# Performance work log

Hardware: AMD Instinct MI355X
Metric: run time of the kernel (lower is better)

Reference implementation:

```python
import jax, jax.numpy as jnp
import numpy as np

D = 256          # input_size
RNN = 256        # rnn_hidden
COND = 64        # cond_dim
HID = 128        # MLP hidden
N_FIXED = 128    # mask.sum() with alternating mask
N_FREE = D - N_FIXED
B = 131072

# Static index arrays implementing the boolean mask (even indices fixed).
IDX_FIXED = np.arange(0, D, 2)
IDX_FREE = np.arange(1, D, 2)


def setup_inputs() -> dict:
    key = jax.random.key(0)
    ks = jax.random.split(key, 8)
    in_dim = N_FIXED + RNN + COND  # 448
    x = jax.random.normal(ks[0], (B, D), jnp.float32)
    h = jax.random.normal(ks[1], (B, RNN + COND), jnp.float32)
    W1 = jax.random.normal(ks[2], (in_dim, HID), jnp.float32) / np.sqrt(in_dim)
    b1 = jnp.zeros((HID,), jnp.float32)
    W2 = jax.random.normal(ks[3], (HID, HID), jnp.float32) / np.sqrt(HID)
    b2 = jnp.zeros((HID,), jnp.float32)
    W3 = jax.random.normal(ks[4], (HID, N_FREE * 2), jnp.float32) / np.sqrt(HID)
    b3 = jnp.zeros((N_FREE * 2,), jnp.float32)
    return {"x": x, "h": h, "W1": W1, "b1": b1, "W2": W2, "b2": b2, "W3": W3, "b3": b3}


def reference(x, h, W1, b1, W2, b2, W3, b3):
    # gather fixed / free halves (static index gather == boolean-mask select)
    x_fixed = x[:, IDX_FIXED]          # [B, N_FIXED]
    x_free = x[:, IDX_FREE]            # [B, N_FREE]
    z = jnp.concatenate([x_fixed, h], axis=-1)  # [B, 448]
    a = jax.nn.relu(z @ W1 + b1)
    a = jax.nn.relu(a @ W2 + b2)
    st = a @ W3 + b3                   # [B, 2*N_FREE]
    s = jnp.tanh(st[:, :N_FREE])
    t = st[:, N_FREE:]
    y_free = x_free * jnp.exp(s) + t
    log_det = jnp.sum(s, axis=-1)
    # scatter-write back into output layout
    y = jnp.zeros_like(x).at[:, IDX_FIXED].set(x_fixed).at[:, IDX_FREE].set(y_free)
    return y, log_det
```

## Files before the change

kernel.cpp:

```cpp
#include <hip/hip_runtime.h>
#include <hip/hip_bf16.h>
#include <stdint.h>

typedef __attribute__((ext_vector_type(8))) short bf16x8;
typedef __attribute__((ext_vector_type(4))) float f32x4;

#define B_ROWS 131072
#define BM 16
#define NT 16
#define GRID 512

#define XB 16384
#define HB 20480
#define H_OFF 32768
#define A1_OFF 73728
#define LSUM_OFF 78080
#define LDS_TOTAL 78336
#define AP 136

#define W1P_OFF 0
#define W2P_OFF 7168
#define W3P_OFF 9216

typedef const __attribute__((address_space(1))) unsigned int gu32;
typedef __attribute__((address_space(3))) unsigned int lu32;

__device__ inline void gl_lds16(const void* g, void* l) {
  __builtin_amdgcn_global_load_lds((gu32*)g, (lu32*)l, 16, 0, 0);
}

__device__ inline uint16_t f2bf(float x) {
  uint32_t u = __float_as_uint(x);
  u += 0x7fffu + ((u >> 16) & 1u);
  return (uint16_t)(u >> 16);
}

__device__ inline float tanh_fast(float x) {
  x = fminf(fmaxf(x, -15.f), 15.f);
  float e = __expf(2.f * x);
  return (e - 1.f) / (e + 1.f);
}

__global__ void prepack_kernel(const float* __restrict__ W1,
                               const float* __restrict__ W2,
                               const float* __restrict__ W3,
                               uint4* __restrict__ wp) {
  int tid = blockIdx.x * 256 + threadIdx.x;
  if (tid >= 13312) return;
  int l = tid & 63, f = tid >> 6;
  const float* W; int N, kt, nt;
  if (f < 112)      { W = W1; N = 128; int ff = f;       nt = ff / 14; kt = ff - nt * 14; }
  else if (f < 144) { W = W2; N = 128; int ff = f - 112; nt = ff >> 2; kt = ff & 3; }
  else              { W = W3; N = 256; int ff = f - 144; nt = ff >> 2; kt = ff & 3; }
  int k0  = kt * 32 + (l >> 4) * 8;
  int col = nt * 16 + (l & 15);
  uint16_t v[8];
#pragma unroll
  for (int j = 0; j < 8; j++) v[j] = f2bf(W[(size_t)(k0 + j) * N + col]);
  uint4 o;
  o.x = (uint32_t)v[0] | ((uint32_t)v[1] << 16);
  o.y = (uint32_t)v[2] | ((uint32_t)v[3] << 16);
  o.z = (uint32_t)v[4] | ((uint32_t)v[5] << 16);
  o.w = (uint32_t)v[6] | ((uint32_t)v[7] << 16);
  wp[tid] = o;
}

__global__ __launch_bounds__(256, 2) void fused_kernel(
    const float* __restrict__ x, const float* __restrict__ h,
    const float* __restrict__ b1, const float* __restrict__ b2,
    const float* __restrict__ b3, const uint4* __restrict__ wp,
    float* __restrict__ y, float* __restrict__ ldet) {
  extern __shared__ uint8_t smem[];
  uint16_t* a1   = (uint16_t*)(smem + A1_OFF);
  float*    lsum = (float*)(smem + LSUM_OFF);

  const int t = threadIdx.x;
  const int wid = t >> 6, l = t & 63;
  const int lr = l & 15, lq = l >> 4;
  const int tile0 = blockIdx.x * NT;

  int xoff[4], hoff[5];
#pragma unroll
  for (int k = 0; k < 4; k++) {
    int r = wid * 4 + k;
    int c = (l & ~15) | ((l & 15) ^ (r & 15));
    xoff[k] = r * 256 + c * 4;
  }
#pragma unroll
  for (int k = 0; k < 5; k++) {
    int s = (wid * 5 + k) * 64 + l;
    int r = s / 80, cp = s - r * 80;
    int c = (cp & ~15) | ((cp & 15) ^ (r & 15));
    hoff[k] = r * 320 + c * 4;
  }

  {
    const float* xg = x + (size_t)(tile0 * BM) * 256;
    const float* hg = h + (size_t)(tile0 * BM) * 320;
#pragma unroll
    for (int k = 0; k < 4; k++)
      gl_lds16(xg + xoff[k], smem + (wid * 4 + k) * 1024);
#pragma unroll
    for (int k = 0; k < 5; k++)
      gl_lds16(hg + hoff[k], smem + H_OFF + (wid * 5 + k) * 1024);
  }

  int cur = 0;
  for (int it = 0; it < NT; ++it) {
    const int m0 = (tile0 + it) * BM;
    __syncthreads();

    const uint8_t* xsc = smem + cur * XB;
    const uint8_t* hsc = smem + H_OFF + cur * HB;
    uint16_t* a2 = (uint16_t*)(smem + H_OFF + cur * HB);

    if (it + 1 < NT) {
      const float* xg = x + (size_t)(m0 + BM) * 256;
      const float* hg = h + (size_t)(m0 + BM) * 320;
      uint8_t* xd = smem + (cur ^ 1) * XB;
      uint8_t* hd = smem + H_OFF + (cur ^ 1) * HB;
#pragma unroll
      for (int k = 0; k < 4; k++)
        gl_lds16(xg + xoff[k], xd + (wid * 4 + k) * 1024);
#pragma unroll
      for (int k = 0; k < 5; k++)
        gl_lds16(hg + hoff[k], hd + (wid * 5 + k) * 1024);
    }

    {
      f32x4 acc[2] = {};
#pragma unroll
      for (int kt = 0; kt < 4; kt++) {
        union { bf16x8 v; __hip_bfloat162 h2[4]; } u;
#pragma unroll
        for (int i = 0; i < 4; i++) {
          int slot = kt * 16 + ((lq * 4 + i) ^ lr);
          float4 q = *(const float4*)(xsc + lr * 1024 + slot * 16);
          u.h2[i] = __float22bfloat162_rn(make_float2(q.x, q.z));
        }
        bf16x8 bfr0 = *(const bf16x8*)&wp[W1P_OFF + ((wid * 2 + 0) * 14 + kt) * 64 + l];
        bf16x8 bfr1 = *(const bf16x8*)&wp[W1P_OFF + ((wid * 2 + 1) * 14 + kt) * 64 + l];
        acc[0] = __builtin_amdgcn_mfma_f32_16x16x32_bf16(u.v, bfr0, acc[0], 0, 0, 0);
        acc[1] = __builtin_amdgcn_mfma_f32_16x16x32_bf16(u.v, bfr1, acc[1], 0, 0, 0);
      }
#pragma unroll 2
      for (int kh = 0; kh < 10; kh++) {
        int c0 = kh * 8 + lq * 2;
        int qd = c0 & ~15, mm = c0 & 15;
        float4 a = *(const float4*)(hsc + lr * 1280 + (qd | (mm ^ lr)) * 16);
        float4 b = *(const float4*)(hsc + lr * 1280 + (qd | ((mm + 1) ^ lr)) * 16);
        union { bf16x8 v; __hip_bfloat162 h2[4]; } u;
        u.h2[0] = __float22bfloat162_rn(make_float2(a.x, a.y));
        u.h2[1] = __float22bfloat162_rn(make_float2(a.z, a.w));
        u.h2[2] = __float22bfloat162_rn(make_float2(b.x, b.y));
        u.h2[3] = __float22bfloat162_rn(make_float2(b.z, b.w));
        int kt = kh + 4;
        bf16x8 bfr0 = *(const bf16x8*)&wp[W1P_OFF + ((wid * 2 + 0) * 14 + kt) * 64 + l];
        bf16x8 bfr1 = *(const bf16x8*)&wp[W1P_OFF + ((wid * 2 + 1) * 14 + kt) * 64 + l];
        acc[0] = __builtin_amdgcn_mfma_f32_16x16x32_bf16(u.v, bfr0, acc[0], 0, 0, 0);
        acc[1] = __builtin_amdgcn_mfma_f32_16x16x32_bf16(u.v, bfr1, acc[1], 0, 0, 0);
      }
#pragma unroll
      for (int nj = 0; nj < 2; nj++) {
        int col = wid * 32 + nj * 16 + lr;
        float bv = b1[col];
#pragma unroll
        for (int r = 0; r < 4; r++)
          a1[(lq * 4 + r) * AP + col] = f2bf(fmaxf(acc[nj][r] + bv, 0.f));
      }
    }
    __syncthreads();

    {
      f32x4 acc[2] = {};
#pragma unroll
      for (int kt = 0; kt < 4; kt++) {
        bf16x8 afr = *(const bf16x8*)&a1[lr * AP + kt * 32 + lq * 8];
        bf16x8 bfr0 = *(const bf16x8*)&wp[W2P_OFF + ((wid * 2 + 0) * 4 + kt) * 64 + l];
        bf16x8 bfr1 = *(const bf16x8*)&wp[W2P_OFF + ((wid * 2 + 1) * 4 + kt) * 64 + l];
        acc[0] = __builtin_amdgcn_mfma_f32_16x16x32_bf16(afr, bfr0, acc[0], 0, 0, 0);
        acc[1] = __builtin_amdgcn_mfma_f32_16x16x32_bf16(afr, bfr1, acc[1], 0, 0, 0);
      }
#pragma unroll
      for (int nj = 0; nj < 2; nj++) {
        int col = wid * 32 + nj * 16 + lr;
        float bv = b2[col];
#pragma unroll
        for (int r = 0; r < 4; r++)
          a2[(lq * 4 + r) * AP + col] = f2bf(fmaxf(acc[nj][r] + bv, 0.f));
      }
    }
    __syncthreads();

    f32x4 acc3[4] = {};
#pragma unroll
    for (int kt = 0; kt < 4; kt++) {
      bf16x8 afr = *(const bf16x8*)&a2[lr * AP + kt * 32 + lq * 8];
      bf16x8 bfrS0 = *(const bf16x8*)&wp[W3P_OFF + ((wid * 2 + 0) * 4 + kt) * 64 + l];
      bf16x8 bfrS1 = *(const bf16x8*)&wp[W3P_OFF + ((wid * 2 + 1) * 4 + kt) * 64 + l];
      bf16x8 bfrT0 = *(const bf16x8*)&wp[W3P_OFF + ((8 + wid * 2 + 0) * 4 + kt) * 64 + l];
      bf16x8 bfrT1 = *(const bf16x8*)&wp[W3P_OFF + ((8 + wid * 2 + 1) * 4 + kt) * 64 + l];
      acc3[0] = __builtin_amdgcn_mfma_f32_16x16x32_bf16(afr, bfrS0, acc3[0], 0, 0, 0);
      acc3[1] = __builtin_amdgcn_mfma_f32_16x16x32_bf16(afr, bfrS1, acc3[1], 0, 0, 0);
      acc3[2] = __builtin_amdgcn_mfma_f32_16x16x32_bf16(afr, bfrT0, acc3[2], 0, 0, 0);
      acc3[3] = __builtin_amdgcn_mfma_f32_16x16x32_bf16(afr, bfrT1, acc3[3], 0, 0, 0);
    }

    float lp[4] = {0.f, 0.f, 0.f, 0.f};
#pragma unroll
    for (int nj = 0; nj < 2; nj++) {
      int colc = wid * 32 + nj * 16 + lr;
      float bs = b3[colc];
      float bt = b3[128 + colc];
#pragma unroll
      for (int r = 0; r < 4; r++) {
        int lrow = lq * 4 + r;
        float sv = tanh_fast(acc3[nj][r] + bs);
        float tv = acc3[nj + 2][r] + bt;
        lp[r] += sv;
        int cch = wid * 16 + nj * 8 + (lr >> 1);
        int slot = (cch & ~15) | ((cch & 15) ^ lrow);
        const float2 xv = *(const float2*)(xsc + lrow * 1024 + slot * 16 + (lr & 1) * 8);
        float2 o;
        o.x = xv.x;
        o.y = xv.y * __expf(sv) + tv;
        *(float2*)(y + (size_t)(m0 + lrow) * 256 + 2 * colc) = o;
      }
    }

#pragma unroll
    for (int r = 0; r < 4; r++) {
      float v = lp[r];
      v += __shfl_xor(v, 1);
      v += __shfl_xor(v, 2);
      v += __shfl_xor(v, 4);
      v += __shfl_xor(v, 8);
      if (lr == 0) lsum[wid * BM + lq * 4 + r] = v;
    }
    __syncthreads();
    if (t < BM)
      ldet[m0 + t] = lsum[t] + lsum[BM + t] + lsum[2 * BM + t] + lsum[3 * BM + t];

    cur ^= 1;
  }
}

extern "C" void kernel_launch(void* const* d_in, const int* in_sizes, int n_in,
                              void* d_out, int out_size, void* d_ws, size_t ws_size,
                              hipStream_t stream) {
  const float* x  = (const float*)d_in[0];
  const float* h  = (const float*)d_in[1];
  const float* W1 = (const float*)d_in[2];
  const float* b1 = (const float*)d_in[3];
  const float* W2 = (const float*)d_in[4];
  const float* b2 = (const float*)d_in[5];
  const float* W3 = (const float*)d_in[6];
  const float* b3 = (const float*)d_in[7];
  float* y    = (float*)d_out;
  float* ldet = y + (size_t)B_ROWS * 256;
  uint4* wp   = (uint4*)d_ws;

  prepack_kernel<<<52, 256, 0, stream>>>(W1, W2, W3, wp);

  (void)hipFuncSetAttribute((const void*)fused_kernel,
                            hipFuncAttributeMaxDynamicSharedMemorySize, LDS_TOTAL);
  fused_kernel<<<GRID, 256, LDS_TOTAL, stream>>>(x, h, b1, b2, b3, wp, y, ldet);
}
```

Measured before the change: 131.1 us.

## Use 8 waves per block with register-resident weights and bf16-staged h tiles

Doubles the block to 512 threads so each wave owns a 16-column slice, and keeps its W1/W2/W3 bf16 fragments in registers instead of reloading them from global memory every tile. The h tile is no longer copied directly into LDS; threads load it, convert it to bf16 and store it into a padded layout, which halves its LDS footprint and removes the per-MFMA conversion. The x tile now uses padded rows instead of an XOR swizzle, and a2 gets its own buffer. In exchange, register pressure rises (about 26 bf16x8 fragments per lane) and the h prefetch becomes a synchronous register round trip placed after the first barrier rather than an asynchronous load.

Measured after the change: 173.0 us. 32.0% more time.

```diff
diff --git a/kernel.cpp b/kernel.cpp
--- a/kernel.cpp
+++ b/kernel.cpp
@@ -10,12 +10,15 @@
 #define NT 16
 #define GRID 512
 
-#define XB 16384
-#define HB 20480
-#define H_OFF 32768
-#define A1_OFF 73728
-#define LSUM_OFF 78080
-#define LDS_TOTAL 78336
+#define XPITCH 1040
+#define XB (16 * XPITCH)
+#define HPITCH 656
+#define HB (16 * HPITCH)
+#define H_OFF (2 * XB)
+#define A1_OFF (H_OFF + 2 * HB)
+#define A2_OFF (A1_OFF + 16 * 272)
+#define LSUM_OFF (A2_OFF + 16 * 272)
+#define LDS_TOTAL (LSUM_OFF + 128 * 4)
 #define AP 136
 
 #define W1P_OFF 0
@@ -65,13 +68,23 @@
   wp[tid] = o;
 }
 
-__global__ __launch_bounds__(256, 2) void fused_kernel(
+__device__ inline void stage_h_chunk(uint8_t* hd, const float* hg, int j) {
+  int row = j / 80, c4 = j - row * 80;
+  float4 v = *(const float4*)(hg + 4 * j);
+  uint2 p;
+  p.x = (uint32_t)f2bf(v.x) | ((uint32_t)f2bf(v.y) << 16);
+  p.y = (uint32_t)f2bf(v.z) | ((uint32_t)f2bf(v.w) << 16);
+  *(uint2*)(hd + row * HPITCH + c4 * 8) = p;
+}
+
+__global__ __launch_bounds__(512, 2) void fused_kernel(
     const float* __restrict__ x, const float* __restrict__ h,
     const float* __restrict__ b1, const float* __restrict__ b2,
     const float* __restrict__ b3, const uint4* __restrict__ wp,
     float* __restrict__ y, float* __restrict__ ldet) {
   extern __shared__ uint8_t smem[];
   uint16_t* a1   = (uint16_t*)(smem + A1_OFF);
+  uint16_t* a2   = (uint16_t*)(smem + A2_OFF);
   float*    lsum = (float*)(smem + LSUM_OFF);
 
   const int t = threadIdx.x;
@@ -79,153 +92,116 @@
   const int lr = l & 15, lq = l >> 4;
   const int tile0 = blockIdx.x * NT;
 
-  int xoff[4], hoff[5];
-#pragma unroll
-  for (int k = 0; k < 4; k++) {
-    int r = wid * 4 + k;
-    int c = (l & ~15) | ((l & 15) ^ (r & 15));
-    xoff[k] = r * 256 + c * 4;
+  bf16x8 w1[14], w2[4], w3s[4], w3t[4];
+#pragma unroll
+  for (int kt = 0; kt < 14; kt++)
+    w1[kt] = *(const bf16x8*)&wp[W1P_OFF + (wid * 14 + kt) * 64 + l];
+#pragma unroll
+  for (int kt = 0; kt < 4; kt++) {
+    w2[kt]  = *(const bf16x8*)&wp[W2P_OFF + (wid * 4 + kt) * 64 + l];
+    w3s[kt] = *(const bf16x8*)&wp[W3P_OFF + (wid * 4 + kt) * 64 + l];
+    w3t[kt] = *(const bf16x8*)&wp[W3P_OFF + ((wid + 8) * 4 + kt) * 64 + l];
   }
-#pragma unroll
-  for (int k = 0; k < 5; k++) {
-    int s = (wid * 5 + k) * 64 + l;
-    int r = s / 80, cp = s - r * 80;
-    int c = (cp & ~15) | ((cp & 15) ^ (r & 15));
-    hoff[k] = r * 320 + c * 4;
-  }
+  const int colc = wid * 16 + lr;
+  const float b1v = b1[colc], b2v = b2[colc];
+  const float b3sv = b3[colc], b3tv = b3[128 + colc];
 
   {
     const float* xg = x + (size_t)(tile0 * BM) * 256;
     const float* hg = h + (size_t)(tile0 * BM) * 320;
 #pragma unroll
-    for (int k = 0; k < 4; k++)
-      gl_lds16(xg + xoff[k], smem + (wid * 4 + k) * 1024);
-#pragma unroll
-    for (int k = 0; k < 5; k++)
-      gl_lds16(hg + hoff[k], smem + H_OFF + (wid * 5 + k) * 1024);
+    for (int k = 0; k < 2; k++) {
+      int r = wid * 2 + k;
+      gl_lds16(xg + r * 256 + l * 4, smem + r * XPITCH);
+    }
+    stage_h_chunk(smem + H_OFF, hg, t);
+    stage_h_chunk(smem + H_OFF, hg, t + 512);
+    if (t < 256) stage_h_chunk(smem + H_OFF, hg, t + 1024);
   }
 
   int cur = 0;
   for (int it = 0; it < NT; ++it) {
     const int m0 = (tile0 + it) * BM;
+    const bool pf = (it + 1 < NT);
     __syncthreads();
 
     const uint8_t* xsc = smem + cur * XB;
     const uint8_t* hsc = smem + H_OFF + cur * HB;
-    uint16_t* a2 = (uint16_t*)(smem + H_OFF + cur * HB);
-
-    if (it + 1 < NT) {
+
+    if (pf) {
       const float* xg = x + (size_t)(m0 + BM) * 256;
-      const float* hg = h + (size_t)(m0 + BM) * 320;
       uint8_t* xd = smem + (cur ^ 1) * XB;
-      uint8_t* hd = smem + H_OFF + (cur ^ 1) * HB;
-#pragma unroll
-      for (int k = 0; k < 4; k++)
-        gl_lds16(xg + xoff[k], xd + (wid * 4 + k) * 1024);
-#pragma unroll
-      for (int k = 0; k < 5; k++)
-        gl_lds16(hg + hoff[k], hd + (wid * 5 + k) * 1024);
+#pragma unroll
+      for (int k = 0; k < 2; k++) {
+        int r = wid * 2 + k;
+        gl_lds16(xg + r * 256 + l * 4, xd + r * XPITCH);
+      }
     }
 
     {
-      f32x4 acc[2] = {};
+      f32x4 acc = {};
 #pragma unroll
       for (int kt = 0; kt < 4; kt++) {
         union { bf16x8 v; __hip_bfloat162 h2[4]; } u;
 #pragma unroll
         for (int i = 0; i < 4; i++) {
-          int slot = kt * 16 + ((lq * 4 + i) ^ lr);
-          float4 q = *(const float4*)(xsc + lr * 1024 + slot * 16);
+          float4 q = *(const float4*)(xsc + lr * XPITCH + kt * 256 + lq * 64 + i * 16);
           u.h2[i] = __float22bfloat162_rn(make_float2(q.x, q.z));
         }
-        bf16x8 bfr0 = *(const bf16x8*)&wp[W1P_OFF + ((wid * 2 + 0) * 14 + kt) * 64 + l];
-        bf16x8 bfr1 = *(const bf16x8*)&wp[W1P_OFF + ((wid * 2 + 1) * 14 + kt) * 64 + l];
-        acc[0] = __builtin_amdgcn_mfma_f32_16x16x32_bf16(u.v, bfr0, acc[0], 0, 0, 0);
-        acc[1] = __builtin_amdgcn_mfma_f32_16x16x32_bf16(u.v, bfr1, acc[1], 0, 0, 0);
-      }
-#pragma unroll 2
+        acc = __builtin_amdgcn_mfma_f32_16x16x32_bf16(u.v, w1[kt], acc, 0, 0, 0);
+      }
+#pragma unroll
       for (int kh = 0; kh < 10; kh++) {
-        int c0 = kh * 8 + lq * 2;
-        int qd = c0 & ~15, mm = c0 & 15;
-        float4 a = *(const float4*)(hsc + lr * 1280 + (qd | (mm ^ lr)) * 16);
-        float4 b = *(const float4*)(hsc + lr * 1280 + (qd | ((mm + 1) ^ lr)) * 16);
-        union { bf16x8 v; __hip_bfloat162 h2[4]; } u;
-        u.h2[0] = __float22bfloat162_rn(make_float2(a.x, a.y));
-        u.h2[1] = __float22bfloat162_rn(make_float2(a.z, a.w));
-        u.h2[2] = __float22bfloat162_rn(make_float2(b.x, b.y));
-        u.h2[3] = __float22bfloat162_rn(make_float2(b.z, b.w));
-        int kt = kh + 4;
-        bf16x8 bfr0 = *(const bf16x8*)&wp[W1P_OFF + ((wid * 2 + 0) * 14 + kt) * 64 + l];
-        bf16x8 bfr1 = *(const bf16x8*)&wp[W1P_OFF + ((wid * 2 + 1) * 14 + kt) * 64 + l];
-        acc[0] = __builtin_amdgcn_mfma_f32_16x16x32_bf16(u.v, bfr0, acc[0], 0, 0, 0);
-        acc[1] = __builtin_amdgcn_mfma_f32_16x16x32_bf16(u.v, bfr1, acc[1], 0, 0, 0);
-      }
-#pragma unroll
-      for (int nj = 0; nj < 2; nj++) {
-        int col = wid * 32 + nj * 16 + lr;
-        float bv = b1[col];
-#pragma unroll
-        for (int r = 0; r < 4; r++)
-          a1[(lq * 4 + r) * AP + col] = f2bf(fmaxf(acc[nj][r] + bv, 0.f));
-      }
-    }
-    __syncthreads();
+        bf16x8 afr = *(const bf16x8*)(hsc + lr * HPITCH + (kh * 32 + lq * 8) * 2);
+        acc = __builtin_amdgcn_mfma_f32_16x16x32_bf16(afr, w1[4 + kh], acc, 0, 0, 0);
+      }
+#pragma unroll
+      for (int r = 0; r < 4; r++)
+        a1[(lq * 4 + r) * AP + colc] = f2bf(fmaxf(acc[r] + b1v, 0.f));
+    }
+    __syncthreads();
+
+    if (pf) {
+      const float* hg = h + (size_t)(m0 + BM) * 320;
+      uint8_t* hd = smem + H_OFF + (cur ^ 1) * HB;
+      stage_h_chunk(hd, hg, t);
+      stage_h_chunk(hd, hg, t + 512);
+      if (t < 256) stage_h_chunk(hd, hg, t + 1024);
+    }
 
     {
-      f32x4 acc[2] = {};
+      f32x4 acc = {};
 #pragma unroll
       for (int kt = 0; kt < 4; kt++) {
         bf16x8 afr = *(const bf16x8*)&a1[lr * AP + kt * 32 + lq * 8];
-        bf16x8 bfr0 = *(const bf16x8*)&wp[W2P_OFF + ((wid * 2 + 0) * 4 + kt) * 64 + l];
-        bf16x8 bfr1 = *(const bf16x8*)&wp[W2P_OFF + ((wid * 2 + 1) * 4 + kt) * 64 + l];
-        acc[0] = __builtin_amdgcn_mfma_f32_16x16x32_bf16(afr, bfr0, acc[0], 0, 0, 0);
-        acc[1] = __builtin_amdgcn_mfma_f32_16x16x32_bf16(afr, bfr1, acc[1], 0, 0, 0);
-      }
-#pragma unroll
-      for (int nj = 0; nj < 2; nj++) {
-        int col = wid * 32 + nj * 16 + lr;
-        float bv = b2[col];
-#pragma unroll
-        for (int r = 0; r < 4; r++)
-          a2[(lq * 4 + r) * AP + col] = f2bf(fmaxf(acc[nj][r] + bv, 0.f));
-      }
-    }
-    __syncthreads();
-
-    f32x4 acc3[4] = {};
+        acc = __builtin_amdgcn_mfma_f32_16x16x32_bf16(afr, w2[kt], acc, 0, 0, 0);
+      }
+#pragma unroll
+      for (int r = 0; r < 4; r++)
+        a2[(lq * 4 + r) * AP + colc] = f2bf(fmaxf(acc[r] + b2v, 0.f));
+    }
+    __syncthreads();
+
+    f32x4 accS = {}, accT = {};
 #pragma unroll
     for (int kt = 0; kt < 4; kt++) {
       bf16x8 afr = *(const bf16x8*)&a2[lr * AP + kt * 32 + lq * 8];
-      bf16x8 bfrS0 = *(const bf16x8*)&wp[W3P_OFF + ((wid * 2 + 0) * 4 + kt) * 64 + l];
-      bf16x8 bfrS1 = *(const bf16x8*)&wp[W3P_OFF + ((wid * 2 + 1) * 4 + kt) * 64 + l];
-      bf16x8 bfrT0 = *(const bf16x8*)&wp[W3P_OFF + ((8 + wid * 2 + 0) * 4 + kt) * 64 + l];
-      bf16x8 bfrT1 = *(const bf16x8*)&wp[W3P_OFF + ((8 + wid * 2 + 1) * 4 + kt) * 64 + l];
-      acc3[0] = __builtin_amdgcn_mfma_f32_16x16x32_bf16(afr, bfrS0, acc3[0], 0, 0, 0);
-      acc3[1] = __builtin_amdgcn_mfma_f32_16x16x32_bf16(afr, bfrS1, acc3[1], 0, 0, 0);
-      acc3[2] = __builtin_amdgcn_mfma_f32_16x16x32_bf16(afr, bfrT0, acc3[2], 0, 0, 0);
-      acc3[3] = __builtin_amdgcn_mfma_f32_16x16x32_bf16(afr, bfrT1, acc3[3], 0, 0, 0);
-    }
-
-    float lp[4] = {0.f, 0.f, 0.f, 0.f};
-#pragma unroll
-    for (int nj = 0; nj < 2; nj++) {
-      int colc = wid * 32 + nj * 16 + lr;
-      float bs = b3[colc];
-      float bt = b3[128 + colc];
-#pragma unroll
-      for (int r = 0; r < 4; r++) {
-        int lrow = lq * 4 + r;
-        float sv = tanh_fast(acc3[nj][r] + bs);
-        float tv = acc3[nj + 2][r] + bt;
-        lp[r] += sv;
-        int cch = wid * 16 + nj * 8 + (lr >> 1);
-        int slot = (cch & ~15) | ((cch & 15) ^ lrow);
-        const float2 xv = *(const float2*)(xsc + lrow * 1024 + slot * 16 + (lr & 1) * 8);
-        float2 o;
-        o.x = xv.x;
-        o.y = xv.y * __expf(sv) + tv;
-        *(float2*)(y + (size_t)(m0 + lrow) * 256 + 2 * colc) = o;
-      }
+      accS = __builtin_amdgcn_mfma_f32_16x16x32_bf16(afr, w3s[kt], accS, 0, 0, 0);
+      accT = __builtin_amdgcn_mfma_f32_16x16x32_bf16(afr, w3t[kt], accT, 0, 0, 0);
+    }
+
+    float lp[4];
+#pragma unroll
+    for (int r = 0; r < 4; r++) {
+      int lrow = lq * 4 + r;
+      float sv = tanh_fast(accS[r] + b3sv);
+      float tv = accT[r] + b3tv;
+      lp[r] = sv;
+      const float2 xv = *(const float2*)(xsc + lrow * XPITCH + colc * 8);
+      float2 o;
+      o.x = xv.x;
+      o.y = xv.y * __expf(sv) + tv;
+      *(float2*)(y + (size_t)(m0 + lrow) * 256 + 2 * colc) = o;
     }
 
 #pragma unroll
@@ -235,12 +211,15 @@
       v += __shfl_xor(v, 2);
       v += __shfl_xor(v, 4);
       v += __shfl_xor(v, 8);
-      if (lr == 0) lsum[wid * BM + lq * 4 + r] = v;
-    }
-    __syncthreads();
-    if (t < BM)
-      ldet[m0 + t] = lsum[t] + lsum[BM + t] + lsum[2 * BM + t] + lsum[3 * BM + t];
-
+      if (lr == 0) lsum[wid * 16 + lq * 4 + r] = v;
+    }
+    __syncthreads();
+    if (t < BM) {
+      float s = 0.f;
+#pragma unroll
+      for (int w = 0; w < 8; w++) s += lsum[w * 16 + t];
+      ldet[m0 + t] = s;
+    }
     cur ^= 1;
   }
 }
@@ -264,5 +243,5 @@
 
   (void)hipFuncSetAttribute((const void*)fused_kernel,
                             hipFuncAttributeMaxDynamicSharedMemorySize, LDS_TOTAL);
-  fused_kernel<<<GRID, 256, LDS_TOTAL, stream>>>(x, h, b1, b2, b3, wp, y, ldet);
-}
+  fused_kernel<<<GRID, 512, LDS_TOTAL, stream>>>(x, h, b1, b2, b3, wp, y, ldet);
+}
```
